# Kernel optimization log

Hardware: AMD Instinct MI355X
Metric: run time of the kernel (lower is better)

The kernel has to match this reference:

```python
import jax, jax.numpy as jnp
import numpy as np

S, K, N, G = 4096, 64, 4096, 512
P = S * K
DIST_BINS = np.array([1, 2, 3, 4, 8, 16, 32, 64], dtype=np.int64)  # 10-bucket distance embedding
PAD_VALUE = 1000.0


def setup_inputs() -> dict:
    key = jax.random.key(0)
    ks = jax.random.split(key, 15)
    return {
        "g_i": jax.random.normal(ks[0], (N, G), dtype=jnp.float32),
        "mention_scores": jax.random.normal(ks[1], (N, 1), dtype=jnp.float32),
        "dist_embed": jax.random.normal(ks[2], (10, 20), dtype=jnp.float32),
        "genre_embed": jax.random.normal(ks[3], (7, 20), dtype=jnp.float32),
        "speaker_embed": jax.random.normal(ks[4], (3, 20), dtype=jnp.float32),
        "W1": jax.random.normal(ks[5], (3 * G + 60, 150), dtype=jnp.float32) * 0.02,
        "b1": jax.random.normal(ks[6], (150,), dtype=jnp.float32) * 0.02,
        "W2": jax.random.normal(ks[7], (150, 1), dtype=jnp.float32) * 0.02,
        "b2": jax.random.normal(ks[8], (1,), dtype=jnp.float32) * 0.02,
        "mention_ids": jax.random.randint(ks[9], (P,), 0, N, dtype=jnp.int64),
        "antecedent_ids": jax.random.randint(ks[10], (P,), 0, N, dtype=jnp.int64),
        "distances": jax.random.randint(ks[11], (P,), 0, 300, dtype=jnp.int64),
        "genres": jax.random.randint(ks[12], (P,), 0, 7, dtype=jnp.int64),
        "speakers": jax.random.randint(ks[13], (P,), 0, 3, dtype=jnp.int64),
        "ant_counts": jax.random.randint(ks[14], (S,), 0, K, dtype=jnp.int64),
    }


def reference(g_i, mention_scores, dist_embed, genre_embed, speaker_embed,
              W1, b1, W2, b2,
              mention_ids, antecedent_ids, distances, genres, speakers, ant_counts):
    # --- phi: distance / genre / speaker embeddings, [P, 60] ---
    buckets = jnp.sum(distances[:, None] >= jnp.asarray(DIST_BINS), axis=1)  # [P] in [0, 8]
    phi = jnp.concatenate(
        [dist_embed[buckets], genre_embed[genres], speaker_embed[speakers]], axis=1)

    # --- pairwise features: (g_i, g_j, g_i * g_j, phi), [P, 3G+60] ---
    i_g = g_i[mention_ids]
    j_g = g_i[antecedent_ids]
    pairs = jnp.concatenate([i_g, j_g, i_g * j_g, phi], axis=1)

    # --- Score MLP: Linear -> ReLU -> Linear, [P, 1] ---
    h = jax.nn.relu(pairs @ W1 + b1)
    s_ij = h @ W2 + b2

    # --- coref score: s_i + s_j + s_ij ---
    coref = mention_scores[mention_ids] + mention_scores[antecedent_ids] + s_ij  # [P, 1]
    scores = coref.reshape(S, K)

    # --- per-span softmax over valid antecedents + epsilon (dummy) column ---
    valid = jnp.arange(K)[None, :] < ant_counts[:, None]            # [S, K]
    logits = jnp.where(valid, scores, -1e9)
    logits = jnp.concatenate([logits, jnp.zeros((S, 1), logits.dtype)], axis=1)  # epsilon = 0
    probs = jax.nn.softmax(logits, axis=1)                          # [S, K+1]

    # pad_and_stack(value=1000): overwrite invalid slots with pad value
    valid_eps = jnp.concatenate([valid, jnp.ones((S, 1), dtype=bool)], axis=1)
    probs = jnp.where(valid_eps, probs, PAD_VALUE)
    return probs
```

## Files before the change

### kernel.cpp

```cpp
#include <hip/hip_runtime.h>

#define NMENT 4096
#define GDIM  512
#define NPAD  160
#define NOUT  150

typedef _Float16 f16x8 __attribute__((ext_vector_type(8)));
typedef _Float16 f16x4 __attribute__((ext_vector_type(4)));
typedef float    f32x4 __attribute__((ext_vector_type(4)));
typedef float    f32x2 __attribute__((ext_vector_type(2)));

#if defined(__has_builtin)
#if __has_builtin(__builtin_amdgcn_cvt_pk_f32_fp8) && __has_builtin(__builtin_amdgcn_cvt_pk_fp8_f32)
#define FP8_HW 1
#endif
#endif

__device__ __forceinline__ float fp8_dec1f(unsigned b) {
    unsigned em = b & 0x7fu;
    unsigned bits = (em < 8u) ? 0u : (((b & 0x80u) << 24) | ((em + 960u) << 20));
    return __builtin_bit_cast(float, bits);
}
__device__ __forceinline__ unsigned fp8_enc1f(float x) {
    float c = fminf(fmaxf(x, -448.f), 448.f);
    unsigned u = __builtin_bit_cast(unsigned, c);
    unsigned s = (u >> 24) & 0x80u;
    unsigned mag = (u & 0x7fffffffu) + 0x80000u;
    int em = (int)(mag >> 20) - 960;
    if (em <= 0) return s;
    if (em > 0x7e) em = 0x7e;
    return s | (unsigned)em;
}
__device__ __forceinline__ f32x2 fp8_dec2_lo(unsigned v) {
#ifdef FP8_HW
    return __builtin_amdgcn_cvt_pk_f32_fp8((int)v, false);
#else
    f32x2 r; r[0] = fp8_dec1f(v & 0xffu); r[1] = fp8_dec1f((v >> 8) & 0xffu); return r;
#endif
}
__device__ __forceinline__ f32x2 fp8_dec2_hi(unsigned v) {
#ifdef FP8_HW
    return __builtin_amdgcn_cvt_pk_f32_fp8((int)v, true);
#else
    f32x2 r; r[0] = fp8_dec1f((v >> 16) & 0xffu); r[1] = fp8_dec1f(v >> 24); return r;
#endif
}
__device__ __forceinline__ unsigned fp8_enc1(float x) {
#ifdef FP8_HW
    return (unsigned)__builtin_amdgcn_cvt_pk_fp8_f32(x, x, 0, false) & 0xffu;
#else
    return fp8_enc1f(x);
#endif
}
__device__ __forceinline__ unsigned fp8_pack4(float a, float b, float c, float d) {
#ifdef FP8_HW
    int v = __builtin_amdgcn_cvt_pk_fp8_f32(a, b, 0, false);
    v = __builtin_amdgcn_cvt_pk_fp8_f32(c, d, v, true);
    return (unsigned)v;
#else
    return fp8_enc1f(a) | (fp8_enc1f(b) << 8) | (fp8_enc1f(c) << 16) | (fp8_enc1f(d) << 24);
#endif
}
__device__ __forceinline__ uint2 fp8_mul8_fp8(uint2 a, uint2 b) {
    f32x2 a0 = fp8_dec2_lo(a.x), a1 = fp8_dec2_hi(a.x);
    f32x2 a2 = fp8_dec2_lo(a.y), a3 = fp8_dec2_hi(a.y);
    f32x2 b0 = fp8_dec2_lo(b.x), b1 = fp8_dec2_hi(b.x);
    f32x2 b2 = fp8_dec2_lo(b.y), b3 = fp8_dec2_hi(b.y);
    f32x2 p0 = a0 * b0, p1 = a1 * b1, p2 = a2 * b2, p3 = a3 * b3;
    uint2 r;
    r.x = fp8_pack4(p0[0], p0[1], p1[0], p1[1]);
    r.y = fp8_pack4(p2[0], p2[1], p3[0], p3[1]);
    return r;
}

#define G8_OFF    0u
#define WABC_OFF  2097152u
#define NODEI_OFF 2342912u
#define NODEJ_OFF 2998272u
#define PHI_OFF   3653632u
#define B1P_OFF   3687232u
#define W2P_OFF   3687872u

__global__ void prep_kernel(const float* __restrict__ g_i,
                            const float* __restrict__ de,
                            const float* __restrict__ ge,
                            const float* __restrict__ se,
                            const float* __restrict__ W1,
                            const float* __restrict__ b1,
                            const float* __restrict__ W2,
                            unsigned char* __restrict__ g8,
                            unsigned char* __restrict__ Wabc8,
                            unsigned char* __restrict__ Phi8,
                            float* __restrict__ b1p,
                            float* __restrict__ W2p)
{
    __shared__ float tl[64 * 152];
    const int b = blockIdx.x, tid = threadIdx.x;

    if (b < 1024) {
        const float4* g4 = (const float4*)g_i;
        int i4 = b * 512 + tid * 2;
        float4 v0 = g4[i4], v1 = g4[i4 + 1];
        unsigned lo = fp8_pack4(v0.x, v0.y, v0.z, v0.w);
        unsigned hi = fp8_pack4(v1.x, v1.y, v1.z, v1.w);
        ((uint2*)g8)[b * 256 + tid] = make_uint2(lo, hi);
    } else if (b < 1048) {
        int b2 = b - 1024, j = b2 >> 3, k0 = (b2 & 7) << 6;
        int rbase = j * 512 + k0;
        for (int idx = tid; idx < 64 * 150; idx += 256) {
            int kk = idx / 150, col = idx - kk * 150;
            tl[kk * 152 + col] = W1[(rbase + kk) * 150 + col];
        }
        __syncthreads();
        for (int idx = tid; idx < 160 * 64; idx += 256) {
            int n = idx >> 6, k = idx & 63;
            float v = (n < 150) ? tl[k * 152 + n] : 0.0f;
            int tile = j * 10 + (n >> 4), c16 = n & 15;
            int kg = k0 + k;
            int ks = kg >> 5, quad = (kg >> 3) & 3, jj = kg & 7;
            Wabc8[(tile * 16 + ks) * 512 + (c16 * 4 + quad) * 8 + jj]
                = (unsigned char)fp8_enc1(v);
        }
    } else if (b < 1180) {
        int e = (b - 1048) * 256 + tid;
        if (e < 210 * 160) {
            int c = e / 160, n = e - c * 160;
            float acc = 0.0f;
            if (n < 150) {
                int bk = c / 21, rest = c - bk * 21, gi = rest / 3, sp = rest - gi * 3;
                #pragma unroll 4
                for (int d = 0; d < 20; ++d) {
                    acc += de[bk * 20 + d] * W1[(1536 + d) * 150 + n];
                    acc += ge[gi * 20 + d] * W1[(1556 + d) * 150 + n];
                    acc += se[sp * 20 + d] * W1[(1576 + d) * 150 + n];
                }
            }
            Phi8[e] = (unsigned char)fp8_enc1(acc);
        }
    } else if (b == 1180) {
        if (tid < 160) b1p[tid] = (tid < 150) ? b1[tid] : 0.0f;
    } else {
        if (tid < 160) W2p[tid] = (tid < 150) ? W2[tid] : 0.0f;
    }
}

__global__ __launch_bounds__(256, 2) void p1_node(
    const unsigned char* __restrict__ g8,
    const unsigned char* __restrict__ Wabc8,
    const float* __restrict__ b1p,
    unsigned char* __restrict__ NodeI8,
    unsigned char* __restrict__ NodeJ8)
{
    __shared__ __align__(16) unsigned char A8s[32 * 528];
    const int tid = threadIdx.x;
    const int lane = tid & 63;
    const int col = lane & 15, quad = lane >> 4;
    const int rowbase = blockIdx.x * 32;

    #pragma unroll
    for (int idx = tid; idx < 32 * 32; idx += 256) {
        int row = idx >> 5, o = (idx & 31) * 16;
        uint4 v = *(const uint4*)(g8 + (rowbase + row) * 512 + o);
        *(uint4*)&A8s[row * 528 + o] = v;
    }
    __syncthreads();

    const int wS = __builtin_amdgcn_readfirstlane(tid >> 6);
    const unsigned char* bbase = Wabc8 + (wS * 5 * 16) * 512 + (col * 4 + quad) * 8;

    f32x4 acc[2][5];
    #pragma unroll
    for (int mt = 0; mt < 2; ++mt)
        #pragma unroll
        for (int tt = 0; tt < 5; ++tt) acc[mt][tt] = f32x4{0.f, 0.f, 0.f, 0.f};

    #pragma unroll 4
    for (int ks = 0; ks < 16; ++ks) {
        long av[2];
        #pragma unroll
        for (int mt = 0; mt < 2; ++mt)
            av[mt] = *(const long*)&A8s[(mt * 16 + col) * 528 + ks * 32 + quad * 8];
        #pragma unroll
        for (int tt = 0; tt < 5; ++tt) {
            long bv = *(const long*)(bbase + (tt * 16 + ks) * 512);
            #pragma unroll
            for (int mt = 0; mt < 2; ++mt)
                acc[mt][tt] = __builtin_amdgcn_mfma_f32_16x16x32_fp8_fp8(
                    av[mt], bv, acc[mt][tt], 0, 0, 0);
        }
    }

    #pragma unroll
    for (int tt = 0; tt < 5; ++tt) {
        int tglob = wS * 5 + tt;
        bool isI = tglob < 10;
        int n = (isI ? tglob : tglob - 10) * 16 + col;
        unsigned char* outp = isI ? NodeI8 : NodeJ8;
        float bias = isI ? b1p[n] : 0.0f;
        #pragma unroll
        for (int mt = 0; mt < 2; ++mt)
            #pragma unroll
            for (int r = 0; r < 4; ++r) {
                int row = rowbase + mt * 16 + quad * 4 + r;
                outp[row * NPAD + n] = (unsigned char)fp8_enc1(acc[mt][tt][r] + bias);
            }
    }
}

__global__ __launch_bounds__(256, 4) void pair_score_kernel(
    const unsigned char* __restrict__ g8,
    const unsigned char* __restrict__ Wc8,
    const unsigned char* __restrict__ NodeI8,
    const unsigned char* __restrict__ NodeJ8,
    const unsigned char* __restrict__ Phi8,
    const float* __restrict__ W2p,
    const float* __restrict__ msc,
    const float* __restrict__ b2,
    const int* __restrict__ mention_ids,
    const int* __restrict__ ant_ids,
    const int* __restrict__ dists,
    const int* __restrict__ genres,
    const int* __restrict__ speakers,
    const int* __restrict__ ant_counts,
    float* __restrict__ out)
{
    __shared__ __align__(16) unsigned char smem[64 * 528];
    __shared__ int   m_lds[64], a_lds[64];
    __shared__ float sc[64];

    const int tid = threadIdx.x, s = blockIdx.x;
    const int lane = tid & 63;
    const int col = lane & 15, quad = lane >> 4;

    if (tid < 64) {
        int p = s * 64 + tid;
        m_lds[tid] = mention_ids[p];
        a_lds[tid] = ant_ids[p];
    }
    __syncthreads();

    #pragma unroll 4
    for (int c = tid; c < 64 * 64; c += 256) {
        int row = c >> 6, ko = (c & 63) * 8;
        uint2 gi = *(const uint2*)(g8 + m_lds[row] * 512 + ko);
        uint2 gj = *(const uint2*)(g8 + a_lds[row] * 512 + ko);
        *(uint2*)&smem[row * 528 + ko] = fp8_mul8_fp8(gi, gj);
    }
    __syncthreads();

    const int wS = __builtin_amdgcn_readfirstlane(tid >> 6);
    const int base = (wS < 2) ? wS * 3 : 6 + (wS - 2) * 2;
    const int cnt  = (wS < 2) ? 3 : 2;
    const int laneoff = (col * 4 + quad) * 8;

    f32x4 acc[4][3];
    #pragma unroll
    for (int mt = 0; mt < 4; ++mt)
        #pragma unroll
        for (int tt = 0; tt < 3; ++tt) acc[mt][tt] = f32x4{0.f, 0.f, 0.f, 0.f};

    const unsigned char* bbase = Wc8 + base * 16 * 512 + laneoff;

    #pragma unroll 4
    for (int ks = 0; ks < 16; ++ks) {
        long av[4];
        #pragma unroll
        for (int mt = 0; mt < 4; ++mt)
            av[mt] = *(const long*)&smem[(mt * 16 + col) * 528 + ks * 32 + quad * 8];
        #pragma unroll
        for (int tt = 0; tt < 3; ++tt) {
            if (tt < cnt) {
                long bv = *(const long*)(bbase + (tt * 16 + ks) * 512);
                #pragma unroll
                for (int mt = 0; mt < 4; ++mt)
                    acc[mt][tt] = __builtin_amdgcn_mfma_f32_16x16x32_fp8_fp8(
                        av[mt], bv, acc[mt][tt], 0, 0, 0);
            }
        }
    }
    __syncthreads();

    _Float16* CLDS16 = (_Float16*)smem;
    #pragma unroll
    for (int tt = 0; tt < 3; ++tt) {
        if (tt < cnt) {
            #pragma unroll
            for (int mt = 0; mt < 4; ++mt)
                #pragma unroll
                for (int r = 0; r < 4; ++r)
                    CLDS16[(mt * 16 + quad * 4 + r) * 168 + (base + tt) * 16 + col]
                        = (_Float16)acc[mt][tt][r];
        }
    }
    __syncthreads();

    const int pe = tid >> 2, q = tid & 3;
    const int pp = s * 64 + pe;
    const int me = m_lds[pe], ae = a_lds[pe];
    const int d = dists[pp];
    const int bk = (d>=1)+(d>=2)+(d>=3)+(d>=4)+(d>=8)+(d>=16)+(d>=32)+(d>=64);
    const int ce = (bk * 7 + genres[pp]) * 3 + speakers[pp];

    const unsigned* NI = (const unsigned*)(NodeI8 + me * NPAD) + q * 10;
    const unsigned* NJ = (const unsigned*)(NodeJ8 + ae * NPAD) + q * 10;
    const unsigned* PH = (const unsigned*)(Phi8 + ce * NPAD) + q * 10;
    const _Float16* crow = CLDS16 + pe * 168 + q * 40;
    const float* w2r = W2p + q * 40;

    float sum = 0.0f;
    #pragma unroll
    for (int i = 0; i < 10; ++i) {
        unsigned ni = NI[i], nj = NJ[i], ph = PH[i];
        f16x4 cf4 = *(const f16x4*)(crow + i * 4);
        float4 wf = *(const float4*)(w2r + i * 4);
        f32x2 ni0 = fp8_dec2_lo(ni), ni1 = fp8_dec2_hi(ni);
        f32x2 nj0 = fp8_dec2_lo(nj), nj1 = fp8_dec2_hi(nj);
        f32x2 ph0 = fp8_dec2_lo(ph), ph1 = fp8_dec2_hi(ph);
        sum += fmaxf((float)cf4[0] + ni0[0] + nj0[0] + ph0[0], 0.0f) * wf.x;
        sum += fmaxf((float)cf4[1] + ni0[1] + nj0[1] + ph0[1], 0.0f) * wf.y;
        sum += fmaxf((float)cf4[2] + ni1[0] + nj1[0] + ph1[0], 0.0f) * wf.z;
        sum += fmaxf((float)cf4[3] + ni1[1] + nj1[1] + ph1[1], 0.0f) * wf.w;
    }
    sum += __shfl_xor(sum, 1);
    sum += __shfl_xor(sum, 2);
    if (q == 0) sc[pe] = sum;
    __syncthreads();

    if (tid < 64) {
        int cnt2 = ant_counts[s];
        bool valid = tid < cnt2;
        float logit = valid
            ? (sc[tid] + msc[m_lds[tid]] + msc[a_lds[tid]] + b2[0])
            : -1e30f;
        float mx = logit;
        mx = fmaxf(mx, __shfl_xor(mx, 1));  mx = fmaxf(mx, __shfl_xor(mx, 2));
        mx = fmaxf(mx, __shfl_xor(mx, 4));  mx = fmaxf(mx, __shfl_xor(mx, 8));
        mx = fmaxf(mx, __shfl_xor(mx, 16)); mx = fmaxf(mx, __shfl_xor(mx, 32));
        mx = fmaxf(mx, 0.0f);
        float e = __expf(logit - mx);
        float ssum = e;
        ssum += __shfl_xor(ssum, 1);  ssum += __shfl_xor(ssum, 2);
        ssum += __shfl_xor(ssum, 4);  ssum += __shfl_xor(ssum, 8);
        ssum += __shfl_xor(ssum, 16); ssum += __shfl_xor(ssum, 32);
        float eps = __expf(-mx);
        ssum += eps;
        float* orow = out + s * 65;
        orow[tid] = valid ? (e / ssum) : 1000.0f;
        if (tid == 0) orow[64] = eps / ssum;
    }
}

extern "C" void kernel_launch(void* const* d_in, const int* in_sizes, int n_in,
                              void* d_out, int out_size, void* d_ws, size_t ws_size,
                              hipStream_t stream)
{
    const float* g_i = (const float*)d_in[0];
    const float* msc = (const float*)d_in[1];
    const float* de  = (const float*)d_in[2];
    const float* ge  = (const float*)d_in[3];
    const float* se  = (const float*)d_in[4];
    const float* W1  = (const float*)d_in[5];
    const float* b1  = (const float*)d_in[6];
    const float* W2  = (const float*)d_in[7];
    const float* b2  = (const float*)d_in[8];
    const int* mid  = (const int*)d_in[9];
    const int* aid  = (const int*)d_in[10];
    const int* dst  = (const int*)d_in[11];
    const int* gen  = (const int*)d_in[12];
    const int* spk  = (const int*)d_in[13];
    const int* cnts = (const int*)d_in[14];

    char* ws = (char*)d_ws;
    unsigned char* g8    = (unsigned char*)(ws + G8_OFF);
    unsigned char* Wabc8 = (unsigned char*)(ws + WABC_OFF);
    unsigned char* NodeI = (unsigned char*)(ws + NODEI_OFF);
    unsigned char* NodeJ = (unsigned char*)(ws + NODEJ_OFF);
    unsigned char* Phi8  = (unsigned char*)(ws + PHI_OFF);
    float*         b1p   = (float*)(ws + B1P_OFF);
    float*         W2p   = (float*)(ws + W2P_OFF);

    prep_kernel<<<dim3(1182), dim3(256), 0, stream>>>(
        g_i, de, ge, se, W1, b1, W2, g8, Wabc8, Phi8, b1p, W2p);

    p1_node<<<dim3(128), dim3(256), 0, stream>>>(
        g8, Wabc8, b1p, NodeI, NodeJ);

    pair_score_kernel<<<dim3(4096), dim3(256), 0, stream>>>(
        g8, Wabc8 + 20 * 16 * 512, NodeI, NodeJ, Phi8, W2p, msc, b2,
        mid, aid, dst, gen, spk, cnts, (float*)d_out);
}
```

Before: 170.6 us.

## Split pair-score K loop into halves to cut LDS and raise occupancy

The pair-score kernel now gathers the g_i*g_j fp8 product in two K-halves, so LDS per block drops from 64x528 to 64x336 bytes, and launch bounds go from 4 to 7 blocks per CU. Each gather thread loads 16 bytes instead of 8, and the epilogue reads NodeI/NodeJ/Phi as uint2 instead of 32-bit words. The W1 reorder in the prep kernel is spread over 96 smaller blocks instead of 24. The aim is more waves resident to hide gather latency, at the cost of an extra barrier pair per block and possible register pressure or spills under the tighter launch bound.

```diff
diff --git a/kernel.cpp b/kernel.cpp
--- a/kernel.cpp
+++ b/kernel.cpp
@@ -94,7 +94,7 @@
                             float* __restrict__ b1p,
                             float* __restrict__ W2p)
 {
-    __shared__ float tl[64 * 152];
+    __shared__ float tl[16 * 152];
     const int b = blockIdx.x, tid = threadIdx.x;
 
     if (b < 1024) {
@@ -104,25 +104,26 @@
         unsigned lo = fp8_pack4(v0.x, v0.y, v0.z, v0.w);
         unsigned hi = fp8_pack4(v1.x, v1.y, v1.z, v1.w);
         ((uint2*)g8)[b * 256 + tid] = make_uint2(lo, hi);
-    } else if (b < 1048) {
-        int b2 = b - 1024, j = b2 >> 3, k0 = (b2 & 7) << 6;
-        int rbase = j * 512 + k0;
-        for (int idx = tid; idx < 64 * 150; idx += 256) {
+    } else if (b < 1120) {
+        int b2 = b - 1024;
+        int sec = b2 >> 5, strip = b2 & 31;
+        int rbase = sec * 512 + strip * 16;
+        for (int idx = tid; idx < 16 * 150; idx += 256) {
             int kk = idx / 150, col = idx - kk * 150;
             tl[kk * 152 + col] = W1[(rbase + kk) * 150 + col];
         }
         __syncthreads();
-        for (int idx = tid; idx < 160 * 64; idx += 256) {
-            int n = idx >> 6, k = idx & 63;
+        for (int idx = tid; idx < 160 * 16; idx += 256) {
+            int n = idx >> 4, k = idx & 15;
             float v = (n < 150) ? tl[k * 152 + n] : 0.0f;
-            int tile = j * 10 + (n >> 4), c16 = n & 15;
-            int kg = k0 + k;
+            int tile = sec * 10 + (n >> 4), c16 = n & 15;
+            int kg = strip * 16 + k;
             int ks = kg >> 5, quad = (kg >> 3) & 3, jj = kg & 7;
             Wabc8[(tile * 16 + ks) * 512 + (c16 * 4 + quad) * 8 + jj]
                 = (unsigned char)fp8_enc1(v);
         }
-    } else if (b < 1180) {
-        int e = (b - 1048) * 256 + tid;
+    } else if (b < 1252) {
+        int e = (b - 1120) * 256 + tid;
         if (e < 210 * 160) {
             int c = e / 160, n = e - c * 160;
             float acc = 0.0f;
@@ -137,7 +138,7 @@
             }
             Phi8[e] = (unsigned char)fp8_enc1(acc);
         }
-    } else if (b == 1180) {
+    } else if (b == 1252) {
         if (tid < 160) b1p[tid] = (tid < 150) ? b1[tid] : 0.0f;
     } else {
         if (tid < 160) W2p[tid] = (tid < 150) ? W2[tid] : 0.0f;
@@ -207,7 +208,7 @@
     }
 }
 
-__global__ __launch_bounds__(256, 4) void pair_score_kernel(
+__global__ __launch_bounds__(256, 7) void pair_score_kernel(
     const unsigned char* __restrict__ g8,
     const unsigned char* __restrict__ Wc8,
     const unsigned char* __restrict__ NodeI8,
@@ -224,7 +225,7 @@
     const int* __restrict__ ant_counts,
     float* __restrict__ out)
 {
-    __shared__ __align__(16) unsigned char smem[64 * 528];
+    __shared__ __align__(16) unsigned char smem[64 * 336];
     __shared__ int   m_lds[64], a_lds[64];
     __shared__ float sc[64];
 
@@ -239,19 +240,11 @@
     }
     __syncthreads();
 
-    #pragma unroll 4
-    for (int c = tid; c < 64 * 64; c += 256) {
-        int row = c >> 6, ko = (c & 63) * 8;
-        uint2 gi = *(const uint2*)(g8 + m_lds[row] * 512 + ko);
-        uint2 gj = *(const uint2*)(g8 + a_lds[row] * 512 + ko);
-        *(uint2*)&smem[row * 528 + ko] = fp8_mul8_fp8(gi, gj);
-    }
-    __syncthreads();
-
     const int wS = __builtin_amdgcn_readfirstlane(tid >> 6);
     const int base = (wS < 2) ? wS * 3 : 6 + (wS - 2) * 2;
     const int cnt  = (wS < 2) ? 3 : 2;
     const int laneoff = (col * 4 + quad) * 8;
+    const unsigned char* bbase = Wc8 + base * 16 * 512 + laneoff;
 
     f32x4 acc[4][3];
     #pragma unroll
@@ -259,26 +252,41 @@
         #pragma unroll
         for (int tt = 0; tt < 3; ++tt) acc[mt][tt] = f32x4{0.f, 0.f, 0.f, 0.f};
 
-    const unsigned char* bbase = Wc8 + base * 16 * 512 + laneoff;
-
-    #pragma unroll 4
-    for (int ks = 0; ks < 16; ++ks) {
-        long av[4];
-        #pragma unroll
-        for (int mt = 0; mt < 4; ++mt)
-            av[mt] = *(const long*)&smem[(mt * 16 + col) * 528 + ks * 32 + quad * 8];
-        #pragma unroll
-        for (int tt = 0; tt < 3; ++tt) {
-            if (tt < cnt) {
-                long bv = *(const long*)(bbase + (tt * 16 + ks) * 512);
-                #pragma unroll
-                for (int mt = 0; mt < 4; ++mt)
-                    acc[mt][tt] = __builtin_amdgcn_mfma_f32_16x16x32_fp8_fp8(
-                        av[mt], bv, acc[mt][tt], 0, 0, 0);
+    #pragma unroll
+    for (int half = 0; half < 2; ++half) {
+        #pragma unroll
+        for (int k = 0; k < 4; ++k) {
+            int chunk = tid + k * 256;
+            int row = chunk >> 4, ko = (chunk & 15) * 16;
+            const unsigned char* gi8 = g8 + m_lds[row] * 512 + half * 256 + ko;
+            const unsigned char* gj8 = g8 + a_lds[row] * 512 + half * 256 + ko;
+            uint4 gi = *(const uint4*)gi8;
+            uint4 gj = *(const uint4*)gj8;
+            uint2 lo = fp8_mul8_fp8(make_uint2(gi.x, gi.y), make_uint2(gj.x, gj.y));
+            uint2 hi = fp8_mul8_fp8(make_uint2(gi.z, gi.w), make_uint2(gj.z, gj.w));
+            *(uint4*)&smem[row * 272 + ko] = make_uint4(lo.x, lo.y, hi.x, hi.y);
+        }
+        __syncthreads();
+
+        #pragma unroll
+        for (int ksl = 0; ksl < 8; ++ksl) {
+            long av[4];
+            #pragma unroll
+            for (int mt = 0; mt < 4; ++mt)
+                av[mt] = *(const long*)&smem[(mt * 16 + col) * 272 + ksl * 32 + quad * 8];
+            #pragma unroll
+            for (int tt = 0; tt < 3; ++tt) {
+                if (tt < cnt) {
+                    long bv = *(const long*)(bbase + (tt * 16 + half * 8 + ksl) * 512);
+                    #pragma unroll
+                    for (int mt = 0; mt < 4; ++mt)
+                        acc[mt][tt] = __builtin_amdgcn_mfma_f32_16x16x32_fp8_fp8(
+                            av[mt], bv, acc[mt][tt], 0, 0, 0);
+                }
             }
         }
-    }
-    __syncthreads();
+        __syncthreads();
+    }
 
     _Float16* CLDS16 = (_Float16*)smem;
     #pragma unroll
@@ -301,25 +309,34 @@
     const int bk = (d>=1)+(d>=2)+(d>=3)+(d>=4)+(d>=8)+(d>=16)+(d>=32)+(d>=64);
     const int ce = (bk * 7 + genres[pp]) * 3 + speakers[pp];
 
-    const unsigned* NI = (const unsigned*)(NodeI8 + me * NPAD) + q * 10;
-    const unsigned* NJ = (const unsigned*)(NodeJ8 + ae * NPAD) + q * 10;
-    const unsigned* PH = (const unsigned*)(Phi8 + ce * NPAD) + q * 10;
+    const uint2* NI = (const uint2*)(NodeI8 + me * NPAD + q * 40);
+    const uint2* NJ = (const uint2*)(NodeJ8 + ae * NPAD + q * 40);
+    const uint2* PH = (const uint2*)(Phi8 + ce * NPAD + q * 40);
     const _Float16* crow = CLDS16 + pe * 168 + q * 40;
     const float* w2r = W2p + q * 40;
 
     float sum = 0.0f;
     #pragma unroll
-    for (int i = 0; i < 10; ++i) {
-        unsigned ni = NI[i], nj = NJ[i], ph = PH[i];
-        f16x4 cf4 = *(const f16x4*)(crow + i * 4);
-        float4 wf = *(const float4*)(w2r + i * 4);
-        f32x2 ni0 = fp8_dec2_lo(ni), ni1 = fp8_dec2_hi(ni);
-        f32x2 nj0 = fp8_dec2_lo(nj), nj1 = fp8_dec2_hi(nj);
-        f32x2 ph0 = fp8_dec2_lo(ph), ph1 = fp8_dec2_hi(ph);
-        sum += fmaxf((float)cf4[0] + ni0[0] + nj0[0] + ph0[0], 0.0f) * wf.x;
-        sum += fmaxf((float)cf4[1] + ni0[1] + nj0[1] + ph0[1], 0.0f) * wf.y;
-        sum += fmaxf((float)cf4[2] + ni1[0] + nj1[0] + ph1[0], 0.0f) * wf.z;
-        sum += fmaxf((float)cf4[3] + ni1[1] + nj1[1] + ph1[1], 0.0f) * wf.w;
+    for (int i = 0; i < 5; ++i) {
+        uint2 ni = NI[i], nj = NJ[i], ph = PH[i];
+        f16x4 c0 = *(const f16x4*)(crow + i * 8);
+        f16x4 c1 = *(const f16x4*)(crow + i * 8 + 4);
+        float4 w0 = *(const float4*)(w2r + i * 8);
+        float4 w1 = *(const float4*)(w2r + i * 8 + 4);
+        f32x2 niA = fp8_dec2_lo(ni.x), niB = fp8_dec2_hi(ni.x);
+        f32x2 niC = fp8_dec2_lo(ni.y), niD = fp8_dec2_hi(ni.y);
+        f32x2 njA = fp8_dec2_lo(nj.x), njB = fp8_dec2_hi(nj.x);
+        f32x2 njC = fp8_dec2_lo(nj.y), njD = fp8_dec2_hi(nj.y);
+        f32x2 phA = fp8_dec2_lo(ph.x), phB = fp8_dec2_hi(ph.x);
+        f32x2 phC = fp8_dec2_lo(ph.y), phD = fp8_dec2_hi(ph.y);
+        sum += fmaxf((float)c0[0] + niA[0] + njA[0] + phA[0], 0.0f) * w0.x;
+        sum += fmaxf((float)c0[1] + niA[1] + njA[1] + phA[1], 0.0f) * w0.y;
+        sum += fmaxf((float)c0[2] + niB[0] + njB[0] + phB[0], 0.0f) * w0.z;
+        sum += fmaxf((float)c0[3] + niB[1] + njB[1] + phB[1], 0.0f) * w0.w;
+        sum += fmaxf((float)c1[0] + niC[0] + njC[0] + phC[0], 0.0f) * w1.x;
+        sum += fmaxf((float)c1[1] + niC[1] + njC[1] + phC[1], 0.0f) * w1.y;
+        sum += fmaxf((float)c1[2] + niD[0] + njD[0] + phD[0], 0.0f) * w1.z;
+        sum += fmaxf((float)c1[3] + niD[1] + njD[1] + phD[1], 0.0f) * w1.w;
     }
     sum += __shfl_xor(sum, 1);
     sum += __shfl_xor(sum, 2);
@@ -379,7 +396,7 @@
     float*         b1p   = (float*)(ws + B1P_OFF);
     float*         W2p   = (float*)(ws + W2P_OFF);
 
-    prep_kernel<<<dim3(1182), dim3(256), 0, stream>>>(
+    prep_kernel<<<dim3(1254), dim3(256), 0, stream>>>(
         g_i, de, ge, se, W1, b1, W2, g8, Wabc8, Phi8, b1p, W2p);
 
     p1_node<<<dim3(128), dim3(256), 0, stream>>>(
```

Result: slower. 240.5 us (+41.0%).
